# Kernel optimization log

Measured on AMD Instinct MI355X. Metric: run time of the kernel, lower is better.

The kernel has to match this reference:

```python
import jax, jax.numpy as jnp
import numpy as np

EPS = 1e-12  # tf.nn.l2_normalize epsilon


def setup_inputs() -> dict:
    key = jax.random.key(0)
    ks = jax.random.split(key, 6)
    B, S, K, D = 256, 512, 20, 256
    encoded_sents = jax.random.normal(ks[0], (B, S, D), dtype=jnp.float32)
    mask = jax.random.randint(ks[1], (B, S), 0, 2) > 0
    keys = jax.random.normal(ks[2], (B, K, D), dtype=jnp.float32)
    scale = 0.05  # truncated-normal-ish init scale for stability
    U = jax.random.normal(ks[3], (D, D), dtype=jnp.float32) * scale
    V = jax.random.normal(ks[4], (D, D), dtype=jnp.float32) * scale
    W = jax.random.normal(ks[5], (D, D), dtype=jnp.float32) * scale
    return {"encoded_sents": encoded_sents, "mask": mask, "keys": keys,
            "U": U, "V": V, "W": W}


def reference(encoded_sents, mask, keys, U, V, W):
    # encoded_sents: [B,S,D], mask: [B,S] bool, keys: [B,K,D], U/V/W: [D,D]
    kV = jnp.einsum('bkd,de->bke', keys, V)  # time-invariant, hoisted

    def step(h, xm):
        x, m = xm                                   # x: [B,D], m: [B] bool
        # gate: sigmoid(sum_d x*(h+k))  -> [B,K]
        g = jax.nn.sigmoid(jnp.einsum('bd,bkd->bk', x, h + keys))
        # candidate: relu(hU + kV + xW)  -> [B,K,D]
        h_tilda = jax.nn.relu(jnp.einsum('bkd,de->bke', h, U) + kV
                              + (x @ W)[:, None, :])
        upd = h + g[..., None] * h_tilda
        # l2 normalize along dim (tf.nn.l2_normalize semantics)
        sq = jnp.sum(upd * upd, axis=2, keepdims=True)
        upd = upd * jax.lax.rsqrt(jnp.maximum(sq, EPS))
        h_new = jnp.where(m[:, None, None], upd, h)
        return h_new, None

    h0 = jnp.zeros_like(keys)
    xs = (jnp.swapaxes(encoded_sents, 0, 1), mask.T)  # [S,B,D], [S,B]
    hT, _ = jax.lax.scan(step, h0, xs)
    return hT  # [B,K,D]
```

## Files before the change

### kernel.cpp

```cpp
#include <hip/hip_runtime.h>
#include <math.h>

#define B_ 256
#define S_ 512
#define K_ 20
#define D_ 256
#define NT 512
#define LDH 264

typedef __attribute__((ext_vector_type(8))) short short8;
typedef __attribute__((ext_vector_type(4))) short short4v;
typedef __attribute__((ext_vector_type(4))) float f32x4;
typedef __attribute__((ext_vector_type(8))) _Float16 half8;
typedef __attribute__((ext_vector_type(2))) __fp16 fp16x2;
typedef __attribute__((ext_vector_type(2))) unsigned int uint2v;

__device__ __forceinline__ unsigned short rne_bf16(float f) {
  unsigned u = __builtin_bit_cast(unsigned, f);
  u += 0x7FFFu + ((u >> 16) & 1u);
  return (unsigned short)(u >> 16);
}
__device__ __forceinline__ float bf16_to_f32(unsigned short h) {
  return __builtin_bit_cast(float, ((unsigned)h) << 16);
}
__device__ __forceinline__ unsigned pk_f16(float a, float b) {
  fp16x2 p = __builtin_amdgcn_cvt_pkrtz(a, b);
  return __builtin_bit_cast(unsigned, p);
}

__global__ __launch_bounds__(NT, 2)
void rnn_fused11(const float* __restrict__ es, const int* __restrict__ mask,
                 const float* __restrict__ keys, const float* __restrict__ U,
                 const float* __restrict__ V, const float* __restrict__ W,
                 float* __restrict__ XWc, float* __restrict__ out) {
  __shared__ unsigned short sH0[32 * LDH];
  __shared__ unsigned short sH1[32 * LDH];
  __shared__ float sRed[2][3][32][12];
  __shared__ short sAct[S_];
  __shared__ int   sNact;

  const int b = blockIdx.x, t = threadIdx.x;
  const int w = t >> 6, lane = t & 63, quad = lane >> 4, n = lane & 15;
  const int e0a = (w << 5) + quad * 4;

  for (int i = t; i < 2 * 3 * 32 * 12; i += NT) ((float*)sRed)[i] = 0.0f;
  if (w == 0) {
    int base = 0;
    for (int c = 0; c < 8; ++c) {
      int s = c * 64 + lane;
      int mv = mask[b * S_ + s];
      unsigned long long bal = __ballot(mv != 0);
      int pos = base + (int)__popcll(bal & ((1ull << lane) - 1ull));
      if (mv) sAct[pos] = (short)s;
      base += (int)__popcll(bal);
    }
    if (lane == 0) sNact = base;
  }
  __syncthreads();
  const int nAct = sNact;

  short8 aHi[8][2], aLo[8][2];
  auto load_A = [&](const float* __restrict__ M) {
#pragma unroll
    for (int kt = 0; kt < 8; ++kt)
#pragma unroll
      for (int et = 0; et < 2; ++et) {
        const int e = ((2 * w + et) << 4) + n;
        const int d0 = kt * 32 + quad * 8;
        short8 h8, l8;
#pragma unroll
        for (int j = 0; j < 8; ++j) {
          float f = M[(d0 + j) * D_ + e];
          unsigned short hi = rne_bf16(f);
          h8[j] = (short)hi;
          l8[j] = (short)rne_bf16(f - bf16_to_f32(hi));
        }
        aHi[kt][et] = h8; aLo[kt][et] = l8;
      }
  };
  auto run_mfma3 = [&](f32x4 acc[2][2]) {
#pragma unroll
    for (int kt = 0; kt < 8; ++kt) {
      short8 bhi[2], blo[2];
#pragma unroll
      for (int ke = 0; ke < 2; ++ke) {
        const int off = (ke * 16 + n) * LDH + kt * 32 + quad * 8;
        bhi[ke] = *(const short8*)&sH0[off];
        blo[ke] = *(const short8*)&sH1[off];
      }
#pragma unroll
      for (int et = 0; et < 2; ++et)
#pragma unroll
        for (int ke = 0; ke < 2; ++ke) {
          acc[et][ke] = __builtin_amdgcn_mfma_f32_16x16x32_bf16(aHi[kt][et], bhi[ke], acc[et][ke], 0, 0, 0);
          acc[et][ke] = __builtin_amdgcn_mfma_f32_16x16x32_bf16(aLo[kt][et], bhi[ke], acc[et][ke], 0, 0, 0);
          acc[et][ke] = __builtin_amdgcn_mfma_f32_16x16x32_bf16(aHi[kt][et], blo[ke], acc[et][ke], 0, 0, 0);
        }
    }
  };

  const size_t bbase = (size_t)b * S_;
  if (nAct > 0) {
    load_A(W);
    const int nPass = (nAct + 31) >> 5;
    for (int p = 0; p < nPass; ++p) {
      {
        const int rr = t >> 4, c0 = (t & 15) * 16;
        const int ridx = p * 32 + rr;
        const int sidx = sAct[(ridx < nAct) ? ridx : (nAct - 1)];
        const float* src = es + ((size_t)b * S_ + sidx) * D_ + c0;
#pragma unroll
        for (int h2 = 0; h2 < 2; ++h2) {
          f32x4 f0 = *(const f32x4*)(src + h2 * 8);
          f32x4 f1 = *(const f32x4*)(src + h2 * 8 + 4);
          short8 hh, ll;
#pragma unroll
          for (int j = 0; j < 4; ++j) {
            unsigned short a = rne_bf16(f0[j]);
            hh[j] = (short)a; ll[j] = (short)rne_bf16(f0[j] - bf16_to_f32(a));
            unsigned short bq = rne_bf16(f1[j]);
            hh[4 + j] = (short)bq; ll[4 + j] = (short)rne_bf16(f1[j] - bf16_to_f32(bq));
          }
          *(short8*)&sH0[rr * LDH + c0 + h2 * 8] = hh;
          *(short8*)&sH1[rr * LDH + c0 + h2 * 8] = ll;
        }
      }
      __syncthreads();
      f32x4 acc[2][2] = {};
      run_mfma3(acc);
#pragma unroll
      for (int et = 0; et < 2; ++et)
#pragma unroll
        for (int ke = 0; ke < 2; ++ke) {
          const int g = p * 32 + ke * 16 + n;
          if (g < nAct)
            *(f32x4*)&XWc[(bbase + g) * D_ + e0a + 16 * et] = acc[et][ke];
        }
      __syncthreads();
    }
  }

  for (int i = t; i < 32 * LDH; i += NT) { sH0[i] = 0; sH1[i] = 0; }
  __syncthreads();

  for (int i = t; i < K_ * D_; i += NT) {
    int k = i >> 8, d = i & 255;
    float f = keys[(b * K_ + k) * D_ + d];
    unsigned short hi = rne_bf16(f);
    sH0[k * LDH + d] = hi;
    sH1[k * LDH + d] = rne_bf16(f - bf16_to_f32(hi));
  }
  f32x4 kReg[2][2];
#pragma unroll
  for (int et = 0; et < 2; ++et)
#pragma unroll
    for (int ke = 0; ke < 2; ++ke) {
      const int k = ke * 16 + n;
#pragma unroll
      for (int r = 0; r < 4; ++r)
        kReg[et][ke][r] = (k < K_) ? keys[(size_t)(b * K_ + k) * D_ + e0a + 16 * et + r] : 0.0f;
    }
  load_A(V);
  __syncthreads();

  f32x4 kvReg[2][2] = {};
  run_mfma3(kvReg);
  __syncthreads();

  for (int i = t; i < K_ * LDH; i += NT) { sH0[i] = 0; sH1[i] = 0; }
  short8 aU[8][2];
#pragma unroll
  for (int kt = 0; kt < 8; ++kt)
#pragma unroll
    for (int et = 0; et < 2; ++et) {
      const int e = ((2 * w + et) << 4) + n;
      const int d0 = kt * 32 + quad * 8;
      short8 h8;
#pragma unroll
      for (int j = 0; j < 8; ++j)
        h8[j] = (short)__builtin_bit_cast(unsigned short, (_Float16)U[(d0 + j) * D_ + e]);
      aU[kt][et] = h8;
    }
  auto run_mfma1 = [&](f32x4 acc[2][2], const unsigned short* __restrict__ bp) {
#pragma unroll
    for (int kt = 0; kt < 8; ++kt) {
      const int co = kt * 32 + quad * 8;
      short8 b0 = *(const short8*)&bp[n * LDH + co];
      short8 b1 = {};
      if (n < 4) b1 = *(const short8*)&bp[(16 + n) * LDH + co];
      half8 q0 = __builtin_bit_cast(half8, b0);
      half8 q1 = __builtin_bit_cast(half8, b1);
#pragma unroll
      for (int et = 0; et < 2; ++et) {
        half8 aq = __builtin_bit_cast(half8, aU[kt][et]);
        acc[et][0] = __builtin_amdgcn_mfma_f32_16x16x32_f16(aq, q0, acc[et][0], 0, 0, 0);
        acc[et][1] = __builtin_amdgcn_mfma_f32_16x16x32_f16(aq, q1, acc[et][1], 0, 0, 0);
      }
    }
  };

  f32x4 hReg[2][2] = {};
  f32x4 xEc[2] = {}, xwEc[2] = {};
  if (nAct > 0) {
    const int s1 = sAct[(nAct > 1) ? 1 : 0];
#pragma unroll
    for (int et = 0; et < 2; ++et) {
      xEc[et]  = *(const f32x4*)&es[((size_t)b * S_ + s1) * D_ + e0a + 16 * et];
      xwEc[et] = *(const f32x4*)&XWc[bbase * D_ + e0a + 16 * et];
    }
    const int s0 = sAct[0];
    float p0 = 0.0f, p1 = 0.0f;
#pragma unroll
    for (int et = 0; et < 2; ++et) {
      f32x4 xq = *(const f32x4*)&es[((size_t)b * S_ + s0) * D_ + e0a + 16 * et];
#pragma unroll
      for (int r = 0; r < 4; ++r) {
        p0 = fmaf(xq[r], kReg[et][0][r], p0);
        p1 = fmaf(xq[r], kReg[et][1][r], p1);
      }
    }
    p0 += __shfl_xor(p0, 16, 64); p0 += __shfl_xor(p0, 32, 64);
    p1 += __shfl_xor(p1, 16, 64); p1 += __shfl_xor(p1, 32, 64);
    if (quad == 0) {
      sRed[0][2][n][w] = p0;
      if (n < 4) sRed[0][2][16 + n][w] = p1;
    }
  }
  __syncthreads();

  auto xswap = [](float& a, float& b) {
    asm("v_permlane32_swap_b32 %0, %1" : "+v"(a), "+v"(b));
  };

  for (int i = 0; i < nAct; ++i) {
    const int rb = i & 1, wbuf = rb ^ 1;
    const unsigned short* bR = rb ? sH1 : sH0;
    unsigned short* bW = rb ? sH0 : sH1;

    const int iX = (i + 2 < nAct) ? i + 2 : nAct - 1;
    const int iW = (i + 1 < nAct) ? i + 1 : nAct - 1;
    const size_t rX = ((size_t)b * S_ + sAct[iX]) * D_;
    f32x4 xEn[2], xwEn[2];
#pragma unroll
    for (int et = 0; et < 2; ++et) {
      xEn[et]  = *(const f32x4*)&es[rX + e0a + 16 * et];
      xwEn[et] = *(const f32x4*)&XWc[(bbase + iW) * D_ + e0a + 16 * et];
    }

    float lmv, gv;
    {
      const int kk = lane & 31;
      f32x4 qa = *(const f32x4*)&sRed[rb][0][kk][0];
      f32x4 qb = *(const f32x4*)&sRed[rb][0][kk][4];
      f32x4 ha = *(const f32x4*)&sRed[rb][1][kk][0];
      f32x4 hb = *(const f32x4*)&sRed[rb][1][kk][4];
      f32x4 ka = *(const f32x4*)&sRed[rb][2][kk][0];
      f32x4 kb = *(const f32x4*)&sRed[rb][2][kk][4];
      f32x4 qs = qa + qb, hs = ha + hb, ks = ka + kb;
      float ss = (qs[0] + qs[1]) + (qs[2] + qs[3]);
      float xh = (hs[0] + hs[1]) + (hs[2] + hs[3]);
      float xk = (ks[0] + ks[1]) + (ks[2] + ks[3]);
      lmv = rsqrtf(fmaxf(ss, 1e-12f));
      gv = __fdividef(1.0f, 1.0f + __expf(-fmaf(lmv, xh, xk)));
    }
    const float lm0 = __builtin_bit_cast(float, __builtin_amdgcn_ds_swizzle(__builtin_bit_cast(int, lmv), 0x000F));
    const float g0  = __builtin_bit_cast(float, __builtin_amdgcn_ds_swizzle(__builtin_bit_cast(int, gv),  0x000F));
    const float lm1s = __builtin_bit_cast(float, __builtin_amdgcn_ds_swizzle(__builtin_bit_cast(int, lmv), 0x0203));
    const float g1s  = __builtin_bit_cast(float, __builtin_amdgcn_ds_swizzle(__builtin_bit_cast(int, gv),  0x0203));
    const float lm1 = (n < 4) ? lm1s : 0.0f;
    const float g1 = (n < 4) ? g1s : 0.0f;

    f32x4 acc[2][2] = {};
    run_mfma1(acc, bR);

    float psq0 = 0.0f, psq1 = 0.0f, pxh0 = 0.0f, pxh1 = 0.0f, pxk0 = 0.0f, pxk1 = 0.0f;
#pragma unroll
    for (int et = 0; et < 2; ++et) {
      const int e0 = e0a + 16 * et;
      f32x4 xw4 = xwEc[et];
      f32x4 xn4 = xEc[et];
      {
        f32x4 u;
#pragma unroll
        for (int r = 0; r < 4; ++r) {
          float T = fmaxf(fmaf(lm0, acc[et][0][r], kvReg[et][0][r] + xw4[r]), 0.0f);
          float uv = fmaf(g0, T, lm0 * hReg[et][0][r]);
          u[r] = uv;
          psq0 = fmaf(uv, uv, psq0);
          pxh0 = fmaf(xn4[r], uv, pxh0);
          pxk0 = fmaf(xn4[r], kReg[et][0][r], pxk0);
        }
        hReg[et][0] = u;
        uint2v hh;
        hh[0] = pk_f16(u[0], u[1]);
        hh[1] = pk_f16(u[2], u[3]);
        *(uint2v*)&bW[n * LDH + e0] = hh;
      }
      {
        f32x4 u;
#pragma unroll
        for (int r = 0; r < 4; ++r) {
          float T = fmaxf(fmaf(lm1, acc[et][1][r], kvReg[et][1][r] + xw4[r]), 0.0f);
          float uv = fmaf(g1, T, lm1 * hReg[et][1][r]);
          u[r] = uv;
          psq1 = fmaf(uv, uv, psq1);
          pxh1 = fmaf(xn4[r], uv, pxh1);
          pxk1 = fmaf(xn4[r], kReg[et][1][r], pxk1);
        }
        hReg[et][1] = u;
        if (n < 4) {
          uint2v hh;
          hh[0] = pk_f16(u[0], u[1]);
          hh[1] = pk_f16(u[2], u[3]);
          *(uint2v*)&bW[(16 + n) * LDH + e0] = hh;
        }
      }
    }
    psq0 += __shfl_xor(psq0, 16, 64); psq1 += __shfl_xor(psq1, 16, 64);
    pxh0 += __shfl_xor(pxh0, 16, 64); pxh1 += __shfl_xor(pxh1, 16, 64);
    pxk0 += __shfl_xor(pxk0, 16, 64); pxk1 += __shfl_xor(pxk1, 16, 64);
    xswap(psq0, psq1); const float sq_s = psq0 + psq1;
    xswap(pxh0, pxh1); const float xh_s = pxh0 + pxh1;
    xswap(pxk0, pxk1); const float xk_s = pxk0 + pxk1;
    if (quad == 0) {
      sRed[wbuf][0][n][w] = sq_s; sRed[wbuf][1][n][w] = xh_s; sRed[wbuf][2][n][w] = xk_s;
    }
    if (quad == 2 && n < 4) {
      sRed[wbuf][0][16 + n][w] = sq_s; sRed[wbuf][1][16 + n][w] = xh_s; sRed[wbuf][2][16 + n][w] = xk_s;
    }
#pragma unroll
    for (int et = 0; et < 2; ++et) { xEc[et] = xEn[et]; xwEc[et] = xwEn[et]; }
    __syncthreads();
  }

  const int fb = nAct & 1;
  float lmF0, lmF1 = 0.0f;
  {
    f32x4 qa = *(const f32x4*)&sRed[fb][0][n][0];
    f32x4 qb = *(const f32x4*)&sRed[fb][0][n][4];
    f32x4 qs = qa + qb;
    lmF0 = rsqrtf(fmaxf((qs[0] + qs[1]) + (qs[2] + qs[3]), 1e-12f));
  }
  if (n < 4) {
    f32x4 qa = *(const f32x4*)&sRed[fb][0][16 + n][0];
    f32x4 qb = *(const f32x4*)&sRed[fb][0][16 + n][4];
    f32x4 qs = qa + qb;
    lmF1 = rsqrtf(fmaxf((qs[0] + qs[1]) + (qs[2] + qs[3]), 1e-12f));
  }
#pragma unroll
  for (int et = 0; et < 2; ++et) {
    const int e0 = e0a + 16 * et;
    {
      f32x4 o;
#pragma unroll
      for (int r = 0; r < 4; ++r) o[r] = lmF0 * hReg[et][0][r];
      *(f32x4*)&out[(size_t)(b * K_ + n) * D_ + e0] = o;
    }
    if (n < 4) {
      f32x4 o;
#pragma unroll
      for (int r = 0; r < 4; ++r) o[r] = lmF1 * hReg[et][1][r];
      *(f32x4*)&out[(size_t)(b * K_ + 16 + n) * D_ + e0] = o;
    }
  }
}

extern "C" void kernel_launch(void* const* d_in, const int* in_sizes, int n_in,
                              void* d_out, int out_size, void* d_ws, size_t ws_size,
                              hipStream_t stream) {
  const float* es   = (const float*)d_in[0];
  const int*   mask = (const int*)d_in[1];
  const float* keys = (const float*)d_in[2];
  const float* U    = (const float*)d_in[3];
  const float* V    = (const float*)d_in[4];
  const float* W    = (const float*)d_in[5];
  float* out = (float*)d_out;
  float* XWc = (float*)d_ws;
  rnn_fused11<<<B_, NT, 0, stream>>>(es, mask, keys, U, V, W, XWc, out);
}
```

Before: 683.9 us.

## Precompute x·key gate terms for all active steps via MFMA prepass into LDS

Adds a prepass in which wave 0 computes x_s·k for every active timestep and all keys using split-bf16 MFMA, storing the results in a new LDS table sXK. The recurrent loop then reads xk from that table instead of accumulating pxk partials, shuffling and reducing them through sRed each step. This removes per-step FMAs, shuffles and LDS traffic from the serial critical path. The cost is an extra pass over the encoded sentences, about 41KB more LDS (which may limit the two-blocks-per-CU occupancy), and wave-0-only work during the prepass.

```diff
diff --git a/kernel.cpp b/kernel.cpp
--- a/kernel.cpp
+++ b/kernel.cpp
@@ -9,7 +9,6 @@
 #define LDH 264
 
 typedef __attribute__((ext_vector_type(8))) short short8;
-typedef __attribute__((ext_vector_type(4))) short short4v;
 typedef __attribute__((ext_vector_type(4))) float f32x4;
 typedef __attribute__((ext_vector_type(8))) _Float16 half8;
 typedef __attribute__((ext_vector_type(2))) __fp16 fp16x2;
@@ -29,13 +28,14 @@
 }
 
 __global__ __launch_bounds__(NT, 2)
-void rnn_fused11(const float* __restrict__ es, const int* __restrict__ mask,
+void rnn_fused12(const float* __restrict__ es, const int* __restrict__ mask,
                  const float* __restrict__ keys, const float* __restrict__ U,
                  const float* __restrict__ V, const float* __restrict__ W,
                  float* __restrict__ XWc, float* __restrict__ out) {
   __shared__ unsigned short sH0[32 * LDH];
   __shared__ unsigned short sH1[32 * LDH];
-  __shared__ float sRed[2][3][32][12];
+  __shared__ float sRed[2][2][32][13];
+  __shared__ float sXK[512 * 20 + 16];
   __shared__ short sAct[S_];
   __shared__ int   sNact;
 
@@ -43,7 +43,7 @@
   const int w = t >> 6, lane = t & 63, quad = lane >> 4, n = lane & 15;
   const int e0a = (w << 5) + quad * 4;
 
-  for (int i = t; i < 2 * 3 * 32 * 12; i += NT) ((float*)sRed)[i] = 0.0f;
+  for (int i = t; i < 2 * 2 * 32 * 13; i += NT) ((float*)sRed)[i] = 0.0f;
   if (w == 0) {
     int base = 0;
     for (int c = 0; c < 8; ++c) {
@@ -78,6 +78,26 @@
         aHi[kt][et] = h8; aLo[kt][et] = l8;
       }
   };
+  auto load_A_keys = [&]() {
+#pragma unroll
+    for (int kt = 0; kt < 8; ++kt)
+#pragma unroll
+      for (int et = 0; et < 2; ++et) {
+        const int kk2 = ((2 * w + et) << 4) + n;
+        const int d0 = kt * 32 + quad * 8;
+        short8 h8 = {}, l8 = {};
+        if (kk2 < K_) {
+#pragma unroll
+          for (int j = 0; j < 8; ++j) {
+            float f = keys[(size_t)(b * K_ + kk2) * D_ + d0 + j];
+            unsigned short hi = rne_bf16(f);
+            h8[j] = (short)hi;
+            l8[j] = (short)rne_bf16(f - bf16_to_f32(hi));
+          }
+        }
+        aHi[kt][et] = h8; aLo[kt][et] = l8;
+      }
+  };
   auto run_mfma3 = [&](f32x4 acc[2][2]) {
 #pragma unroll
     for (int kt = 0; kt < 8; ++kt) {
@@ -98,33 +118,59 @@
         }
     }
   };
+  auto stage_rows = [&](int p) {
+    const int rr = t >> 4, c0 = (t & 15) * 16;
+    const int ridx = p * 32 + rr;
+    const int sidx = sAct[(ridx < nAct) ? ridx : (nAct - 1)];
+    const float* src = es + ((size_t)b * S_ + sidx) * D_ + c0;
+#pragma unroll
+    for (int h2 = 0; h2 < 2; ++h2) {
+      f32x4 f0 = *(const f32x4*)(src + h2 * 8);
+      f32x4 f1 = *(const f32x4*)(src + h2 * 8 + 4);
+      short8 hh, ll;
+#pragma unroll
+      for (int j = 0; j < 4; ++j) {
+        unsigned short a = rne_bf16(f0[j]);
+        hh[j] = (short)a; ll[j] = (short)rne_bf16(f0[j] - bf16_to_f32(a));
+        unsigned short bq = rne_bf16(f1[j]);
+        hh[4 + j] = (short)bq; ll[4 + j] = (short)rne_bf16(f1[j] - bf16_to_f32(bq));
+      }
+      *(short8*)&sH0[rr * LDH + c0 + h2 * 8] = hh;
+      *(short8*)&sH1[rr * LDH + c0 + h2 * 8] = ll;
+    }
+  };
 
   const size_t bbase = (size_t)b * S_;
+  const int nPass = (nAct + 31) >> 5;
+
+  if (nAct > 0) {
+    load_A_keys();
+    for (int p = 0; p < nPass; ++p) {
+      stage_rows(p);
+      __syncthreads();
+      if (w == 0) {
+        f32x4 axk[2][2] = {};
+        run_mfma3(axk);
+#pragma unroll
+        for (int et = 0; et < 2; ++et) {
+          const int kb = et * 16 + quad * 4;
+          if (kb < K_) {
+#pragma unroll
+            for (int ke = 0; ke < 2; ++ke) {
+              const int row = p * 32 + ke * 16 + n;
+              *(f32x4*)&sXK[row * 20 + kb] = axk[et][ke];
+            }
+          }
+        }
+      }
+      __syncthreads();
+    }
+  }
+
   if (nAct > 0) {
     load_A(W);
-    const int nPass = (nAct + 31) >> 5;
     for (int p = 0; p < nPass; ++p) {
-      {
-        const int rr = t >> 4, c0 = (t & 15) * 16;
-        const int ridx = p * 32 + rr;
-        const int sidx = sAct[(ridx < nAct) ? ridx : (nAct - 1)];
-        const float* src = es + ((size_t)b * S_ + sidx) * D_ + c0;
-#pragma unroll
-        for (int h2 = 0; h2 < 2; ++h2) {
-          f32x4 f0 = *(const f32x4*)(src + h2 * 8);
-          f32x4 f1 = *(const f32x4*)(src + h2 * 8 + 4);
-          short8 hh, ll;
-#pragma unroll
-          for (int j = 0; j < 4; ++j) {
-            unsigned short a = rne_bf16(f0[j]);
-            hh[j] = (short)a; ll[j] = (short)rne_bf16(f0[j] - bf16_to_f32(a));
-            unsigned short bq = rne_bf16(f1[j]);
-            hh[4 + j] = (short)bq; ll[4 + j] = (short)rne_bf16(f1[j] - bf16_to_f32(bq));
-          }
-          *(short8*)&sH0[rr * LDH + c0 + h2 * 8] = hh;
-          *(short8*)&sH1[rr * LDH + c0 + h2 * 8] = ll;
-        }
-      }
+      stage_rows(p);
       __syncthreads();
       f32x4 acc[2][2] = {};
       run_mfma3(acc);
@@ -150,16 +196,6 @@
     sH0[k * LDH + d] = hi;
     sH1[k * LDH + d] = rne_bf16(f - bf16_to_f32(hi));
   }
-  f32x4 kReg[2][2];
-#pragma unroll
-  for (int et = 0; et < 2; ++et)
-#pragma unroll
-    for (int ke = 0; ke < 2; ++ke) {
-      const int k = ke * 16 + n;
-#pragma unroll
-      for (int r = 0; r < 4; ++r)
-        kReg[et][ke][r] = (k < K_) ? keys[(size_t)(b * K_ + k) * D_ + e0a + 16 * et + r] : 0.0f;
-    }
   load_A(V);
   __syncthreads();
 
@@ -208,23 +244,6 @@
       xEc[et]  = *(const f32x4*)&es[((size_t)b * S_ + s1) * D_ + e0a + 16 * et];
       xwEc[et] = *(const f32x4*)&XWc[bbase * D_ + e0a + 16 * et];
     }
-    const int s0 = sAct[0];
-    float p0 = 0.0f, p1 = 0.0f;
-#pragma unroll
-    for (int et = 0; et < 2; ++et) {
-      f32x4 xq = *(const f32x4*)&es[((size_t)b * S_ + s0) * D_ + e0a + 16 * et];
-#pragma unroll
-      for (int r = 0; r < 4; ++r) {
-        p0 = fmaf(xq[r], kReg[et][0][r], p0);
-        p1 = fmaf(xq[r], kReg[et][1][r], p1);
-      }
-    }
-    p0 += __shfl_xor(p0, 16, 64); p0 += __shfl_xor(p0, 32, 64);
-    p1 += __shfl_xor(p1, 16, 64); p1 += __shfl_xor(p1, 32, 64);
-    if (quad == 0) {
-      sRed[0][2][n][w] = p0;
-      if (n < 4) sRed[0][2][16 + n][w] = p1;
-    }
   }
   __syncthreads();
 
@@ -254,12 +273,10 @@
       f32x4 qb = *(const f32x4*)&sRed[rb][0][kk][4];
       f32x4 ha = *(const f32x4*)&sRed[rb][1][kk][0];
       f32x4 hb = *(const f32x4*)&sRed[rb][1][kk][4];
-      f32x4 ka = *(const f32x4*)&sRed[rb][2][kk][0];
-      f32x4 kb = *(const f32x4*)&sRed[rb][2][kk][4];
-      f32x4 qs = qa + qb, hs = ha + hb, ks = ka + kb;
+      const float xk = sXK[i * 20 + kk];
+      f32x4 qs = qa + qb, hs = ha + hb;
       float ss = (qs[0] + qs[1]) + (qs[2] + qs[3]);
       float xh = (hs[0] + hs[1]) + (hs[2] + hs[3]);
-      float xk = (ks[0] + ks[1]) + (ks[2] + ks[3]);
       lmv = rsqrtf(fmaxf(ss, 1e-12f));
       gv = __fdividef(1.0f, 1.0f + __expf(-fmaf(lmv, xh, xk)));
     }
@@ -273,7 +290,7 @@
     f32x4 acc[2][2] = {};
     run_mfma1(acc, bR);
 
-    float psq0 = 0.0f, psq1 = 0.0f, pxh0 = 0.0f, pxh1 = 0.0f, pxk0 = 0.0f, pxk1 = 0.0f;
+    float psq0 = 0.0f, psq1 = 0.0f, pxh0 = 0.0f, pxh1 = 0.0f;
 #pragma unroll
     for (int et = 0; et < 2; ++et) {
       const int e0 = e0a + 16 * et;
@@ -288,7 +305,6 @@
           u[r] = uv;
           psq0 = fmaf(uv, uv, psq0);
           pxh0 = fmaf(xn4[r], uv, pxh0);
-          pxk0 = fmaf(xn4[r], kReg[et][0][r], pxk0);
         }
         hReg[et][0] = u;
         uint2v hh;
@@ -305,7 +321,6 @@
           u[r] = uv;
           psq1 = fmaf(uv, uv, psq1);
           pxh1 = fmaf(xn4[r], uv, pxh1);
-          pxk1 = fmaf(xn4[r], kReg[et][1][r], pxk1);
         }
         hReg[et][1] = u;
         if (n < 4) {
@@ -318,15 +333,13 @@
     }
     psq0 += __shfl_xor(psq0, 16, 64); psq1 += __shfl_xor(psq1, 16, 64);
     pxh0 += __shfl_xor(pxh0, 16, 64); pxh1 += __shfl_xor(pxh1, 16, 64);
-    pxk0 += __shfl_xor(pxk0, 16, 64); pxk1 += __shfl_xor(pxk1, 16, 64);
     xswap(psq0, psq1); const float sq_s = psq0 + psq1;
     xswap(pxh0, pxh1); const float xh_s = pxh0 + pxh1;
-    xswap(pxk0, pxk1); const float xk_s = pxk0 + pxk1;
     if (quad == 0) {
-      sRed[wbuf][0][n][w] = sq_s; sRed[wbuf][1][n][w] = xh_s; sRed[wbuf][2][n][w] = xk_s;
+      sRed[wbuf][0][n][w] = sq_s; sRed[wbuf][1][n][w] = xh_s;
     }
     if (quad == 2 && n < 4) {
-      sRed[wbuf][0][16 + n][w] = sq_s; sRed[wbuf][1][16 + n][w] = xh_s; sRed[wbuf][2][16 + n][w] = xk_s;
+      sRed[wbuf][0][16 + n][w] = sq_s; sRed[wbuf][1][16 + n][w] = xh_s;
     }
 #pragma unroll
     for (int et = 0; et < 2; ++et) { xEc[et] = xEn[et]; xwEc[et] = xwEn[et]; }
@@ -376,5 +389,5 @@
   const float* W    = (const float*)d_in[5];
   float* out = (float*)d_out;
   float* XWc = (float*)d_ws;
-  rnn_fused11<<<B_, NT, 0, stream>>>(es, mask, keys, U, V, W, XWc, out);
-}
+  rnn_fused12<<<B_, NT, 0, stream>>>(es, mask, keys, U, V, W, XWc, out);
+}
```

After: 676.6 us. Within noise of the previous version (-1.1%).
